# Performance work log

Measured on AMD Instinct MI355X. Metric: run time of the kernel, lower is better.

The kernel has to match this reference:

```python
import jax, jax.numpy as jnp
import numpy as np

B, T, C, H = 2, 2048, 1024, 16
D = C // H  # head dim


def setup_inputs() -> dict:
    key = jax.random.key(0)
    ks = jax.random.split(key, 10)
    s = 1.0 / np.sqrt(C)  # xavier-ish scale
    inp = {
        "q": jax.random.normal(ks[0], (B, T, C), jnp.float32),
        "k": jax.random.normal(ks[1], (B, T, C), jnp.float32),
        "Wq": jax.random.normal(ks[2], (C, C), jnp.float32) * s,
        "bq": jnp.zeros((C,), jnp.float32),
        "Wk": jax.random.normal(ks[3], (C, C), jnp.float32) * s,
        "bk": jnp.zeros((C,), jnp.float32),
        "Wv": jax.random.normal(ks[4], (C, C), jnp.float32) * s,
        "bv": jnp.zeros((C,), jnp.float32),
        "Wo": jax.random.normal(ks[5], (C, C), jnp.float32) * s,
        "bo": jnp.zeros((C,), jnp.float32),
        # causal mask (lower triangular); masked_fill where mask == 0
        "mask": jnp.tril(jnp.ones((T, T), jnp.int32))[None, None],
    }
    return inp


def reference(q, k, Wq, bq, Wk, bk, Wv, bv, Wo, bo, mask):
    # projections (weights stored input-major: y = x @ W + b)
    qp = q @ Wq + bq                       # [B,T,C]
    kp = k @ Wk + bk                       # [B,T,C]
    vp = kp @ Wv + bv                      # quirk: V computed from projected K

    def heads(x):
        return x.reshape(B, T, H, D).transpose(0, 2, 1, 3)  # [B,H,T,D]

    qh, kh, vh = heads(qp), heads(kp), heads(vp)
    scores = jnp.einsum("bhqd,bhkd->bhqk", qh, kh) / jnp.sqrt(jnp.float32(D))
    scores = jnp.where(mask == 0, -jnp.inf, scores)
    attention_weights = jax.nn.softmax(scores, axis=-1)  # [B,H,T,T]
    # dropout omitted (eval mode / p=0)
    ctx = jnp.einsum("bhqk,bhkd->bhqd", attention_weights, vh)
    ctx = ctx.transpose(0, 2, 1, 3).reshape(B, T, C)
    out = ctx @ Wo + bo
    return out, attention_weights
```

## Files before the change

kernel.cpp:

```cpp
#include <hip/hip_runtime.h>

typedef __attribute__((ext_vector_type(8))) short bf16x8;
typedef __attribute__((ext_vector_type(4))) float f32x4;
typedef unsigned short u16;
typedef unsigned int u32;

#define T_SEQ 2048
#define C_DIM 1024
#define NH 16
#define HD 64
#define BATCH 2

__device__ __forceinline__ u16 f2bf(float f) {
    union { float f; u32 u; } v; v.f = f;
    u32 u = v.u;
    u32 r = (u + 0x7FFFu + ((u >> 16) & 1u)) >> 16;
    return (u16)r;
}

__device__ __forceinline__ float fexp2(float x) { return __builtin_amdgcn_exp2f(x); }

__device__ __forceinline__ float bflo(u32 u) {
    union { u32 u; float f; } v; v.u = u << 16; return v.f;
}
__device__ __forceinline__ float bfhi(u32 u) {
    union { u32 u; float f; } v; v.u = u & 0xFFFF0000u; return v.f;
}

__device__ __forceinline__ void gld_lds16(const void* g, void* l) {
    __builtin_amdgcn_global_load_lds(
        (const __attribute__((address_space(1))) void*)g,
        (__attribute__((address_space(3))) void*)l, 16, 0, 0);
}

__global__ __launch_bounds__(256) void transpose_to_bf16(
    const float* __restrict__ W0, const float* __restrict__ W1,
    const float* __restrict__ W2, const float* __restrict__ W3,
    u16* __restrict__ O0, u16* __restrict__ O1,
    u16* __restrict__ O2, u16* __restrict__ O3)
{
    __shared__ float tile[32][33];
    const float* W = blockIdx.z == 0 ? W0 : blockIdx.z == 1 ? W1 : blockIdx.z == 2 ? W2 : W3;
    u16* O = blockIdx.z == 0 ? O0 : blockIdx.z == 1 ? O1 : blockIdx.z == 2 ? O2 : O3;
    const int tx = threadIdx.x, ty = threadIdx.y;
    const int bx = blockIdx.x * 32, by = blockIdx.y * 32;
#pragma unroll
    for (int i = 0; i < 4; ++i)
        tile[ty + i * 8][tx] = W[(size_t)(by + ty + i * 8) * C_DIM + bx + tx];
    __syncthreads();
#pragma unroll
    for (int i = 0; i < 4; ++i)
        O[(size_t)(bx + ty + i * 8) * C_DIM + by + tx] = f2bf(tile[tx][ty + i * 8]);
}

template<bool XF32, int OMODE>
__global__ __launch_bounds__(256) void gemm_bt(
    const void* __restrict__ X0_, const void* __restrict__ X1_,
    const u16* __restrict__ W0T, const u16* __restrict__ W1T,
    const float* __restrict__ b0_, const float* __restrict__ b1_,
    void* __restrict__ Y0_, void* __restrict__ Y1_,
    int M, int N, int K)
{
    __shared__ u16 As[64 * 32];
    __shared__ u16 Bs[128 * 32];
    const int tid = threadIdx.x;
    const int w = tid >> 6, l = tid & 63;
    const int lr = l & 15, lg = l >> 4;
    const int z = blockIdx.z;
    const void* Xv = z ? X1_ : X0_;
    const u16* WT = z ? W1T : W0T;
    const float* bias = z ? b1_ : b0_;
    void* Yv = z ? Y1_ : Y0_;
    const int m0 = blockIdx.y * 64, n0 = blockIdx.x * 128;
    const int grow = l >> 2, gcol = (l & 3) * 8;
    f32x4 acc[4][2] = {};

    for (int k0 = 0; k0 < K; k0 += 32) {
        __syncthreads();
        if (XF32) {
            const int row = tid >> 2, cg = tid & 3;
            const float* g = (const float*)Xv + (size_t)(m0 + row) * K + k0 + cg * 8;
            float4 a0 = *(const float4*)g;
            float4 a1 = *(const float4*)(g + 4);
            union { u16 h[8]; uint4 q; } pk;
            pk.h[0] = f2bf(a0.x); pk.h[1] = f2bf(a0.y);
            pk.h[2] = f2bf(a0.z); pk.h[3] = f2bf(a0.w);
            pk.h[4] = f2bf(a1.x); pk.h[5] = f2bf(a1.y);
            pk.h[6] = f2bf(a1.z); pk.h[7] = f2bf(a1.w);
            *(uint4*)&As[row * 32 + cg * 8] = pk.q;
        } else {
            gld_lds16((const u16*)Xv + (size_t)(m0 + w * 16 + grow) * K + k0 + gcol,
                      &As[w * 512]);
        }
#pragma unroll
        for (int i = 0; i < 2; ++i)
            gld_lds16(WT + (size_t)(n0 + w * 32 + i * 16 + grow) * K + k0 + gcol,
                      &Bs[(w * 2 + i) * 512]);
        __syncthreads();
        bf16x8 af[4], bfr[2];
#pragma unroll
        for (int i = 0; i < 4; ++i)
            af[i] = *(const bf16x8*)&As[(i * 16 + lr) * 32 + lg * 8];
#pragma unroll
        for (int j = 0; j < 2; ++j)
            bfr[j] = *(const bf16x8*)&Bs[(w * 32 + j * 16 + lr) * 32 + lg * 8];
#pragma unroll
        for (int i = 0; i < 4; ++i)
#pragma unroll
            for (int j = 0; j < 2; ++j)
                acc[i][j] = __builtin_amdgcn_mfma_f32_16x16x32_bf16(af[i], bfr[j], acc[i][j], 0, 0, 0);
    }

#pragma unroll
    for (int i = 0; i < 4; ++i) {
        const int rowb = m0 + i * 16 + lg * 4;
#pragma unroll
        for (int j = 0; j < 2; ++j) {
            const int col = n0 + w * 32 + j * 16 + lr;
            const float bv = bias[col];
            if (OMODE == 2) {
                union { u16 h[4]; uint2 q; } pk;
#pragma unroll
                for (int r = 0; r < 4; ++r) pk.h[r] = f2bf(acc[i][j][r] + bv);
                const int bb = rowb >> 11, tt = rowb & 2047;
                const int hh = col >> 6, dd = col & 63;
                u16* dst = (u16*)Yv + ((size_t)((bb * NH + hh) * HD + dd)) * T_SEQ + tt;
                *(uint2*)dst = pk.q;
            } else {
#pragma unroll
                for (int r = 0; r < 4; ++r) {
                    const float v = acc[i][j][r] + bv;
                    if (OMODE == 1)
                        ((float*)Yv)[(size_t)(rowb + r) * N + col] = v;
                    else
                        ((u16*)Yv)[(size_t)(rowb + r) * N + col] = f2bf(v);
                }
            }
        }
    }
}

#define PV_QS 67
#define PV_WS (16 * PV_QS + 8)

__global__ __launch_bounds__(512, 4) void attn_kernel(
    const u16* __restrict__ qp, const u16* __restrict__ kp,
    const u16* __restrict__ vt, u16* __restrict__ ctx,
    float* __restrict__ attn)
{
    __shared__ float statm[8][16], statl[8][16];
    __shared__ float pvbuf[8 * PV_WS];

    const int tid = threadIdx.x;
    const int w = tid >> 6, l = tid & 63;
    const int lr = l & 15, lg = l >> 4;

    const int wgid = (blockIdx.x & 7) * 512 + (blockIdx.x >> 3);
    const int b = wgid >> 11;
    const int h = (wgid >> 7) & 15;
    const int strip = 127 - (wgid & 127);
    const int q0 = strip * 16;

    const size_t bh_off = (size_t)b * T_SEQ * C_DIM + h * HD;
    const u16* qb = qp + bh_off;
    const u16* kb = kp + bh_off;
    const u16* vtb = vt + ((size_t)(b * NH + h) * HD) * T_SEQ;
    float* ab = attn + (size_t)(b * NH + h) * T_SEQ * T_SEQ;

    const float SC = 0.125f * 1.44269504088896f;
    const float MNEG = -1e30f;

    const int qrow = q0 + lr;
    const int n32 = (q0 + 47) >> 5;

    {
        const int zs = n32 * 32;
        const int row = tid >> 5;
        const int c0 = (tid & 31) * 4;
        float* zr = ab + (size_t)(q0 + row) * T_SEQ;
        const f32x4 z4 = { 0.f, 0.f, 0.f, 0.f };
        for (int c = zs + c0; c < T_SEQ; c += 128)
            __builtin_nontemporal_store(z4, (f32x4*)(zr + c));
    }

    const bf16x8 aq0 = *(const bf16x8*)(qb + (size_t)(q0 + lr) * C_DIM + lg * 8);
    const bf16x8 aq1 = *(const bf16x8*)(qb + (size_t)(q0 + lr) * C_DIM + 32 + lg * 8);

    u32 ec[8][2];
    u32 ec2[8][2];
    float mtj[8], Sj[8];
    float ml = MNEG;
#pragma unroll
    for (int j = 0; j < 8; ++j) {
        const int ti = w + 8 * j;
        if (ti < n32) {
            const int kvb = ti * 32;
            const u16* kr0 = kb + (size_t)(kvb + lr) * C_DIM;
            const u16* kr1 = kb + (size_t)(kvb + 16 + lr) * C_DIM;
            const bf16x8 k00 = *(const bf16x8*)(kr0 + lg * 8);
            const bf16x8 k01 = *(const bf16x8*)(kr0 + 32 + lg * 8);
            const bf16x8 k10 = *(const bf16x8*)(kr1 + lg * 8);
            const bf16x8 k11 = *(const bf16x8*)(kr1 + 32 + lg * 8);
            f32x4 s[2] = {};
            s[0] = __builtin_amdgcn_mfma_f32_16x16x32_bf16(k00, aq0, s[0], 0, 0, 0);
            s[0] = __builtin_amdgcn_mfma_f32_16x16x32_bf16(k01, aq1, s[0], 0, 0, 0);
            s[1] = __builtin_amdgcn_mfma_f32_16x16x32_bf16(k10, aq0, s[1], 0, 0, 0);
            s[1] = __builtin_amdgcn_mfma_f32_16x16x32_bf16(k11, aq1, s[1], 0, 0, 0);
            float sv[2][4];
            float mt = MNEG;
#pragma unroll
            for (int t = 0; t < 2; ++t)
#pragma unroll
                for (int r = 0; r < 4; ++r) {
                    float v = s[t][r] * SC;
                    if (kvb + 16 * t + 4 * lg + r > qrow) v = MNEG;
                    sv[t][r] = v;
                    mt = fmaxf(mt, v);
                }
            mtj[j] = mt;
            float ss = 0.f;
            float e[2][4];
#pragma unroll
            for (int t = 0; t < 2; ++t)
#pragma unroll
                for (int r = 0; r < 4; ++r) {
                    e[t][r] = fexp2(sv[t][r] - mt);
                    ss += e[t][r];
                }
            Sj[j] = ss;
#pragma unroll
            for (int t = 0; t < 2; ++t) {
                ec[j][t]  = (u32)f2bf(e[t][0]) | ((u32)f2bf(e[t][1]) << 16);
                ec2[j][t] = (u32)f2bf(e[t][2]) | ((u32)f2bf(e[t][3]) << 16);
            }
            ml = fmaxf(ml, mt);
        } else {
            mtj[j] = MNEG; Sj[j] = 0.f;
            ec[j][0] = ec[j][1] = ec2[j][0] = ec2[j][1] = 0;
        }
    }
    float ll = 0.f;
#pragma unroll
    for (int j = 0; j < 8; ++j) ll += Sj[j] * fexp2(mtj[j] - ml);
#pragma unroll
    for (int d = 16; d <= 32; d <<= 1) {
        const float mo = __shfl_xor(ml, d);
        const float lo = __shfl_xor(ll, d);
        const float mn = fmaxf(ml, mo);
        ll = ll * fexp2(ml - mn) + lo * fexp2(mo - mn);
        ml = mn;
    }
    if (l < 16) { statm[w][lr] = ml; statl[w][lr] = ll; }
    __syncthreads();

    float mf = MNEG;
#pragma unroll
    for (int ww = 0; ww < 8; ++ww) mf = fmaxf(mf, statm[ww][lr]);
    float lf = 0.f;
#pragma unroll
    for (int ww = 0; ww < 8; ++ww) lf += statl[ww][lr] * fexp2(statm[ww][lr] - mf);
    const float rlf = 1.f / lf;

    f32x4 cacc[4] = {};
#pragma unroll
    for (int j = 0; j < 8; ++j) {
        const int ti = w + 8 * j;
        if (ti < n32) {
            const int kvb = ti * 32;
            bf16x8 vf[4];
#pragma unroll
            for (int dt = 0; dt < 4; ++dt)
                vf[dt] = *(const bf16x8*)(vtb + (size_t)(dt * 16 + lr) * T_SEQ + kvb + lg * 8);
            const float scale = fexp2(mtj[j] - mf) * rlf;
            u32 pw[2][2];
#pragma unroll
            for (int t2 = 0; t2 < 2; ++t2) {
                float p[4];
                p[0] = bflo(ec[j][t2]) * scale;
                p[1] = bfhi(ec[j][t2]) * scale;
                p[2] = bflo(ec2[j][t2]) * scale;
                p[3] = bfhi(ec2[j][t2]) * scale;
                f32x4 pv4 = { p[0], p[1], p[2], p[3] };
                __builtin_nontemporal_store(pv4,
                    (f32x4*)(ab + (size_t)qrow * T_SEQ + kvb + 16 * t2 + 4 * lg));
                pw[t2][0] = (u32)f2bf(p[0]) | ((u32)f2bf(p[1]) << 16);
                pw[t2][1] = (u32)f2bf(p[2]) | ((u32)f2bf(p[3]) << 16);
            }
            const int bl = lr + ((lg & 1) << 5);
            const u32 a0 = (u32)__shfl((int)pw[0][0], bl);
            const u32 a1 = (u32)__shfl((int)pw[0][1], bl);
            const u32 a2 = (u32)__shfl((int)pw[0][0], bl + 16);
            const u32 a3 = (u32)__shfl((int)pw[0][1], bl + 16);
            const u32 b0 = (u32)__shfl((int)pw[1][0], bl);
            const u32 b1 = (u32)__shfl((int)pw[1][1], bl);
            const u32 b2 = (u32)__shfl((int)pw[1][0], bl + 16);
            const u32 b3 = (u32)__shfl((int)pw[1][1], bl + 16);
            const bool hi2 = lg >= 2;
            union { u32 ww[4]; bf16x8 v; } pa;
            pa.ww[0] = hi2 ? b0 : a0;
            pa.ww[1] = hi2 ? b1 : a1;
            pa.ww[2] = hi2 ? b2 : a2;
            pa.ww[3] = hi2 ? b3 : a3;
            __builtin_amdgcn_s_setprio(1);
#pragma unroll
            for (int dt = 0; dt < 4; ++dt)
                cacc[dt] = __builtin_amdgcn_mfma_f32_16x16x32_bf16(pa.v, vf[dt], cacc[dt], 0, 0, 0);
            __builtin_amdgcn_s_setprio(0);
        }
    }

    {
        float* pwv = pvbuf + w * PV_WS;
#pragma unroll
        for (int dt = 0; dt < 4; ++dt)
#pragma unroll
            for (int r = 0; r < 4; ++r)
                pwv[(4 * lg + r) * PV_QS + dt * 16 + lr] = cacc[dt][r];
    }
    __syncthreads();

    {
        const int qq = tid >> 5;
        const int d0 = (tid & 31) * 2;
        float s0 = 0.f, s1 = 0.f;
#pragma unroll
        for (int ww = 0; ww < 8; ++ww) {
            const float* pwv = pvbuf + ww * PV_WS + qq * PV_QS;
            s0 += pwv[d0];
            s1 += pwv[d0 + 1];
        }
        union { u16 hh[2]; u32 u; } pk;
        pk.hh[0] = f2bf(s0); pk.hh[1] = f2bf(s1);
        u16* cb = ctx + bh_off;
        *(u32*)(cb + (size_t)(q0 + qq) * C_DIM + d0) = pk.u;
    }
}

extern "C" void kernel_launch(void* const* d_in, const int* in_sizes, int n_in,
                              void* d_out, int out_size, void* d_ws, size_t ws_size,
                              hipStream_t stream)
{
    const float* q  = (const float*)d_in[0];
    const float* k  = (const float*)d_in[1];
    const float* Wq = (const float*)d_in[2];
    const float* bq = (const float*)d_in[3];
    const float* Wk = (const float*)d_in[4];
    const float* bk = (const float*)d_in[5];
    const float* Wv = (const float*)d_in[6];
    const float* bv = (const float*)d_in[7];
    const float* Wo = (const float*)d_in[8];
    const float* bo = (const float*)d_in[9];
    (void)in_sizes; (void)n_in; (void)out_size; (void)ws_size;

    float* out = (float*)d_out;
    float* attn = out + (size_t)BATCH * T_SEQ * C_DIM;

    const size_t MC = (size_t)BATCH * T_SEQ * C_DIM;
    u16* qp  = (u16*)d_ws;
    u16* kp  = qp + MC;
    u16* vt  = kp + MC;
    u16* ctx = vt + MC;
    u16* WqT = ctx + MC;
    u16* WkT = WqT + (size_t)C_DIM * C_DIM;
    u16* WvT = WkT + (size_t)C_DIM * C_DIM;
    u16* WoT = WvT + (size_t)C_DIM * C_DIM;

    transpose_to_bf16<<<dim3(32, 32, 4), dim3(32, 8), 0, stream>>>(
        Wq, Wk, Wv, Wo, WqT, WkT, WvT, WoT);

    const int M = BATCH * T_SEQ;
    dim3 gqk(C_DIM / 128, M / 64, 2);
    dim3 g1(C_DIM / 128, M / 64, 1);
    gemm_bt<true, 0><<<gqk, 256, 0, stream>>>(q, k, WqT, WkT, bq, bk,
                                              qp, kp, M, C_DIM, C_DIM);
    gemm_bt<false, 2><<<g1, 256, 0, stream>>>(kp, kp, WvT, WvT, bv, bv,
                                              vt, vt, M, C_DIM, C_DIM);

    attn_kernel<<<dim3(4096), 512, 0, stream>>>(qp, kp, vt, ctx, attn);

    gemm_bt<false, 1><<<g1, 256, 0, stream>>>(ctx, ctx, WoT, WoT, bo, bo,
                                              out, out, M, C_DIM, C_DIM);
}
```

Baseline: 254.2 us.

## Double-buffer LDS tiles and widen K-step to 64 in projection GEMM

The projection GEMM now keeps two LDS buffers for the A and B tiles and uses a K-step of 64 instead of 32. The next tile is issued to global (or global-to-LDS) loads before the MFMAs on the current tile, so memory latency overlaps compute, and only one barrier is needed per iteration. This doubles LDS use per block, which may cut occupancy. The wider rows also change the LDS access pattern, which could add bank conflicts on the fragment reads.

Result: slower. 264.7 us (+4.2%).

```diff
diff --git a/kernel.cpp b/kernel.cpp
--- a/kernel.cpp
+++ b/kernel.cpp
@@ -61,8 +61,8 @@
     void* __restrict__ Y0_, void* __restrict__ Y1_,
     int M, int N, int K)
 {
-    __shared__ u16 As[64 * 32];
-    __shared__ u16 Bs[128 * 32];
+    __shared__ u16 As[2][64 * 64];
+    __shared__ u16 Bs[2][128 * 64];
     const int tid = threadIdx.x;
     const int w = tid >> 6, l = tid & 63;
     const int lr = l & 15, lg = l >> 4;
@@ -72,43 +72,85 @@
     const float* bias = z ? b1_ : b0_;
     void* Yv = z ? Y1_ : Y0_;
     const int m0 = blockIdx.y * 64, n0 = blockIdx.x * 128;
-    const int grow = l >> 2, gcol = (l & 3) * 8;
+    const int grow8 = l >> 3;
+    const int gcol8 = (l & 7) * 8;
+    const int rowA = tid >> 2, cgA = tid & 3;
     f32x4 acc[4][2] = {};
 
-    for (int k0 = 0; k0 < K; k0 += 32) {
+    auto stageB = [&](int k0, int buf) {
+#pragma unroll
+        for (int i = 0; i < 4; ++i)
+            gld_lds16(WT + (size_t)(n0 + w * 32 + i * 8 + grow8) * K + k0 + gcol8,
+                      &Bs[buf][(w * 32 + i * 8) * 64]);
+    };
+    auto stageAb = [&](int k0, int buf) {
+#pragma unroll
+        for (int i = 0; i < 2; ++i)
+            gld_lds16((const u16*)Xv + (size_t)(m0 + w * 16 + i * 8 + grow8) * K + k0 + gcol8,
+                      &As[buf][(w * 16 + i * 8) * 64]);
+    };
+
+    if (XF32) {
+        const float* g = (const float*)Xv + (size_t)(m0 + rowA) * K + cgA * 16;
+        float4 a0 = *(const float4*)g;
+        float4 a1 = *(const float4*)(g + 4);
+        float4 a2 = *(const float4*)(g + 8);
+        float4 a3 = *(const float4*)(g + 12);
+        union { u16 h[8]; uint4 q; } p0, p1;
+        p0.h[0] = f2bf(a0.x); p0.h[1] = f2bf(a0.y); p0.h[2] = f2bf(a0.z); p0.h[3] = f2bf(a0.w);
+        p0.h[4] = f2bf(a1.x); p0.h[5] = f2bf(a1.y); p0.h[6] = f2bf(a1.z); p0.h[7] = f2bf(a1.w);
+        p1.h[0] = f2bf(a2.x); p1.h[1] = f2bf(a2.y); p1.h[2] = f2bf(a2.z); p1.h[3] = f2bf(a2.w);
+        p1.h[4] = f2bf(a3.x); p1.h[5] = f2bf(a3.y); p1.h[6] = f2bf(a3.z); p1.h[7] = f2bf(a3.w);
+        *(uint4*)&As[0][rowA * 64 + cgA * 16] = p0.q;
+        *(uint4*)&As[0][rowA * 64 + cgA * 16 + 8] = p1.q;
+    } else {
+        stageAb(0, 0);
+    }
+    stageB(0, 0);
+    __syncthreads();
+
+    int cur = 0;
+    for (int k0 = 0; k0 < K; k0 += 64) {
+        const bool has_next = (k0 + 64 < K);
+        float4 a0, a1, a2, a3;
+        if (has_next) {
+            if (XF32) {
+                const float* g = (const float*)Xv + (size_t)(m0 + rowA) * K + k0 + 64 + cgA * 16;
+                a0 = *(const float4*)g;
+                a1 = *(const float4*)(g + 4);
+                a2 = *(const float4*)(g + 8);
+                a3 = *(const float4*)(g + 12);
+            } else {
+                stageAb(k0 + 64, cur ^ 1);
+            }
+            stageB(k0 + 64, cur ^ 1);
+        }
+#pragma unroll
+        for (int h = 0; h < 2; ++h) {
+            bf16x8 af[4], bfr[2];
+#pragma unroll
+            for (int i = 0; i < 4; ++i)
+                af[i] = *(const bf16x8*)&As[cur][(i * 16 + lr) * 64 + h * 32 + lg * 8];
+#pragma unroll
+            for (int j = 0; j < 2; ++j)
+                bfr[j] = *(const bf16x8*)&Bs[cur][(w * 32 + j * 16 + lr) * 64 + h * 32 + lg * 8];
+#pragma unroll
+            for (int i = 0; i < 4; ++i)
+#pragma unroll
+                for (int j = 0; j < 2; ++j)
+                    acc[i][j] = __builtin_amdgcn_mfma_f32_16x16x32_bf16(af[i], bfr[j], acc[i][j], 0, 0, 0);
+        }
+        if (XF32 && has_next) {
+            union { u16 h[8]; uint4 q; } p0, p1;
+            p0.h[0] = f2bf(a0.x); p0.h[1] = f2bf(a0.y); p0.h[2] = f2bf(a0.z); p0.h[3] = f2bf(a0.w);
+            p0.h[4] = f2bf(a1.x); p0.h[5] = f2bf(a1.y); p0.h[6] = f2bf(a1.z); p0.h[7] = f2bf(a1.w);
+            p1.h[0] = f2bf(a2.x); p1.h[1] = f2bf(a2.y); p1.h[2] = f2bf(a2.z); p1.h[3] = f2bf(a2.w);
+            p1.h[4] = f2bf(a3.x); p1.h[5] = f2bf(a3.y); p1.h[6] = f2bf(a3.z); p1.h[7] = f2bf(a3.w);
+            *(uint4*)&As[cur ^ 1][rowA * 64 + cgA * 16] = p0.q;
+            *(uint4*)&As[cur ^ 1][rowA * 64 + cgA * 16 + 8] = p1.q;
+        }
         __syncthreads();
-        if (XF32) {
-            const int row = tid >> 2, cg = tid & 3;
-            const float* g = (const float*)Xv + (size_t)(m0 + row) * K + k0 + cg * 8;
-            float4 a0 = *(const float4*)g;
-            float4 a1 = *(const float4*)(g + 4);
-            union { u16 h[8]; uint4 q; } pk;
-            pk.h[0] = f2bf(a0.x); pk.h[1] = f2bf(a0.y);
-            pk.h[2] = f2bf(a0.z); pk.h[3] = f2bf(a0.w);
-            pk.h[4] = f2bf(a1.x); pk.h[5] = f2bf(a1.y);
-            pk.h[6] = f2bf(a1.z); pk.h[7] = f2bf(a1.w);
-            *(uint4*)&As[row * 32 + cg * 8] = pk.q;
-        } else {
-            gld_lds16((const u16*)Xv + (size_t)(m0 + w * 16 + grow) * K + k0 + gcol,
-                      &As[w * 512]);
-        }
-#pragma unroll
-        for (int i = 0; i < 2; ++i)
-            gld_lds16(WT + (size_t)(n0 + w * 32 + i * 16 + grow) * K + k0 + gcol,
-                      &Bs[(w * 2 + i) * 512]);
-        __syncthreads();
-        bf16x8 af[4], bfr[2];
-#pragma unroll
-        for (int i = 0; i < 4; ++i)
-            af[i] = *(const bf16x8*)&As[(i * 16 + lr) * 32 + lg * 8];
-#pragma unroll
-        for (int j = 0; j < 2; ++j)
-            bfr[j] = *(const bf16x8*)&Bs[(w * 32 + j * 16 + lr) * 32 + lg * 8];
-#pragma unroll
-        for (int i = 0; i < 4; ++i)
-#pragma unroll
-            for (int j = 0; j < 2; ++j)
-                acc[i][j] = __builtin_amdgcn_mfma_f32_16x16x32_bf16(af[i], bfr[j], acc[i][j], 0, 0, 0);
+        cur ^= 1;
     }
 
 #pragma unroll
```

## Stage attention probabilities in LDS for coalesced stores, contiguous tile ranges per wave

Applied to the files above, without the earlier changes.

Each wave now handles a contiguous range of key tiles instead of a strided set. This lets two adjacent 32-column tiles be staged in shared memory and written to the attention matrix as contiguous 256-byte row segments, replacing the earlier scattered 16-byte stores. The goal is to cut the store-transaction overhead on the large fp32 attention-weights output. In exchange it adds LDS traffic, more shared memory per block (which can lower occupancy), and a possibly less even split of work across waves.

Result: no change. 250.2 us (-1.6%).

```diff
diff --git a/kernel.cpp b/kernel.cpp
--- a/kernel.cpp
+++ b/kernel.cpp
@@ -150,6 +150,7 @@
 {
     __shared__ float statm[8][16], statl[8][16];
     __shared__ float pvbuf[8 * PV_WS];
+    __shared__ float pchunk[8][16][68];
 
     const int tid = threadIdx.x;
     const int w = tid >> 6, l = tid & 63;
@@ -171,10 +172,12 @@
     const float MNEG = -1e30f;
 
     const int qrow = q0 + lr;
-    const int n32 = (q0 + 47) >> 5;
+    const int nt = (q0 + 47) >> 5;
+    const int lo = (w * nt) >> 3;
+    const int hi = ((w + 1) * nt) >> 3;
 
     {
-        const int zs = n32 * 32;
+        const int zs = nt * 32;
         const int row = tid >> 5;
         const int c0 = (tid & 31) * 4;
         float* zr = ab + (size_t)(q0 + row) * T_SEQ;
@@ -191,9 +194,9 @@
     float mtj[8], Sj[8];
     float ml = MNEG;
 #pragma unroll
-    for (int j = 0; j < 8; ++j) {
-        const int ti = w + 8 * j;
-        if (ti < n32) {
+    for (int jj = 0; jj < 8; ++jj) {
+        const int ti = lo + jj;
+        if (ti < hi) {
             const int kvb = ti * 32;
             const u16* kr0 = kb + (size_t)(kvb + lr) * C_DIM;
             const u16* kr1 = kb + (size_t)(kvb + 16 + lr) * C_DIM;
@@ -217,7 +220,7 @@
                     sv[t][r] = v;
                     mt = fmaxf(mt, v);
                 }
-            mtj[j] = mt;
+            mtj[jj] = mt;
             float ss = 0.f;
             float e[2][4];
 #pragma unroll
@@ -227,27 +230,27 @@
                     e[t][r] = fexp2(sv[t][r] - mt);
                     ss += e[t][r];
                 }
-            Sj[j] = ss;
+            Sj[jj] = ss;
 #pragma unroll
             for (int t = 0; t < 2; ++t) {
-                ec[j][t]  = (u32)f2bf(e[t][0]) | ((u32)f2bf(e[t][1]) << 16);
-                ec2[j][t] = (u32)f2bf(e[t][2]) | ((u32)f2bf(e[t][3]) << 16);
+                ec[jj][t]  = (u32)f2bf(e[t][0]) | ((u32)f2bf(e[t][1]) << 16);
+                ec2[jj][t] = (u32)f2bf(e[t][2]) | ((u32)f2bf(e[t][3]) << 16);
             }
             ml = fmaxf(ml, mt);
         } else {
-            mtj[j] = MNEG; Sj[j] = 0.f;
-            ec[j][0] = ec[j][1] = ec2[j][0] = ec2[j][1] = 0;
+            mtj[jj] = MNEG; Sj[jj] = 0.f;
+            ec[jj][0] = ec[jj][1] = ec2[jj][0] = ec2[jj][1] = 0;
         }
     }
     float ll = 0.f;
 #pragma unroll
-    for (int j = 0; j < 8; ++j) ll += Sj[j] * fexp2(mtj[j] - ml);
+    for (int jj = 0; jj < 8; ++jj) ll += Sj[jj] * fexp2(mtj[jj] - ml);
 #pragma unroll
     for (int d = 16; d <= 32; d <<= 1) {
         const float mo = __shfl_xor(ml, d);
-        const float lo = __shfl_xor(ll, d);
+        const float lo2 = __shfl_xor(ll, d);
         const float mn = fmaxf(ml, mo);
-        ll = ll * fexp2(ml - mn) + lo * fexp2(mo - mn);
+        ll = ll * fexp2(ml - mn) + lo2 * fexp2(mo - mn);
         ml = mn;
     }
     if (l < 16) { statm[w][lr] = ml; statl[w][lr] = ll; }
@@ -263,49 +266,77 @@
 
     f32x4 cacc[4] = {};
 #pragma unroll
-    for (int j = 0; j < 8; ++j) {
-        const int ti = w + 8 * j;
-        if (ti < n32) {
-            const int kvb = ti * 32;
-            bf16x8 vf[4];
-#pragma unroll
-            for (int dt = 0; dt < 4; ++dt)
-                vf[dt] = *(const bf16x8*)(vtb + (size_t)(dt * 16 + lr) * T_SEQ + kvb + lg * 8);
-            const float scale = fexp2(mtj[j] - mf) * rlf;
-            u32 pw[2][2];
-#pragma unroll
-            for (int t2 = 0; t2 < 2; ++t2) {
-                float p[4];
-                p[0] = bflo(ec[j][t2]) * scale;
-                p[1] = bfhi(ec[j][t2]) * scale;
-                p[2] = bflo(ec2[j][t2]) * scale;
-                p[3] = bfhi(ec2[j][t2]) * scale;
-                f32x4 pv4 = { p[0], p[1], p[2], p[3] };
-                __builtin_nontemporal_store(pv4,
-                    (f32x4*)(ab + (size_t)qrow * T_SEQ + kvb + 16 * t2 + 4 * lg));
-                pw[t2][0] = (u32)f2bf(p[0]) | ((u32)f2bf(p[1]) << 16);
-                pw[t2][1] = (u32)f2bf(p[2]) | ((u32)f2bf(p[3]) << 16);
+    for (int j0 = 0; j0 < 8; j0 += 2) {
+        int nv = 0;
+#pragma unroll
+        for (int c = 0; c < 2; ++c) {
+            const int jj = j0 + c;
+            const int ti = lo + jj;
+            if (ti < hi) {
+                nv = c + 1;
+                const int kvb = ti * 32;
+                bf16x8 vf[4];
+#pragma unroll
+                for (int dt = 0; dt < 4; ++dt)
+                    vf[dt] = *(const bf16x8*)(vtb + (size_t)(dt * 16 + lr) * T_SEQ + kvb + lg * 8);
+                const float scale = fexp2(mtj[jj] - mf) * rlf;
+                u32 pw[2][2];
+#pragma unroll
+                for (int t2 = 0; t2 < 2; ++t2) {
+                    float p[4];
+                    p[0] = bflo(ec[jj][t2]) * scale;
+                    p[1] = bfhi(ec[jj][t2]) * scale;
+                    p[2] = bflo(ec2[jj][t2]) * scale;
+                    p[3] = bfhi(ec2[jj][t2]) * scale;
+                    f32x4 pv4 = { p[0], p[1], p[2], p[3] };
+                    *(f32x4*)&pchunk[w][lr][c * 32 + 16 * t2 + 4 * lg] = pv4;
+                    pw[t2][0] = (u32)f2bf(p[0]) | ((u32)f2bf(p[1]) << 16);
+                    pw[t2][1] = (u32)f2bf(p[2]) | ((u32)f2bf(p[3]) << 16);
+                }
+                const int bl = lr + ((lg & 1) << 5);
+                const u32 a0 = (u32)__shfl((int)pw[0][0], bl);
+                const u32 a1 = (u32)__shfl((int)pw[0][1], bl);
+                const u32 a2 = (u32)__shfl((int)pw[0][0], bl + 16);
+                const u32 a3 = (u32)__shfl((int)pw[0][1], bl + 16);
+                const u32 b0 = (u32)__shfl((int)pw[1][0], bl);
+                const u32 b1 = (u32)__shfl((int)pw[1][1], bl);
+                const u32 b2 = (u32)__shfl((int)pw[1][0], bl + 16);
+                const u32 b3 = (u32)__shfl((int)pw[1][1], bl + 16);
+                const bool hi2 = lg >= 2;
+                union { u32 ww[4]; bf16x8 v; } pa;
+                pa.ww[0] = hi2 ? b0 : a0;
+                pa.ww[1] = hi2 ? b1 : a1;
+                pa.ww[2] = hi2 ? b2 : a2;
+                pa.ww[3] = hi2 ? b3 : a3;
+                __builtin_amdgcn_s_setprio(1);
+#pragma unroll
+                for (int dt = 0; dt < 4; ++dt)
+                    cacc[dt] = __builtin_amdgcn_mfma_f32_16x16x32_bf16(pa.v, vf[dt], cacc[dt], 0, 0, 0);
+                __builtin_amdgcn_s_setprio(0);
             }
-            const int bl = lr + ((lg & 1) << 5);
-            const u32 a0 = (u32)__shfl((int)pw[0][0], bl);
-            const u32 a1 = (u32)__shfl((int)pw[0][1], bl);
-            const u32 a2 = (u32)__shfl((int)pw[0][0], bl + 16);
-            const u32 a3 = (u32)__shfl((int)pw[0][1], bl + 16);
-            const u32 b0 = (u32)__shfl((int)pw[1][0], bl);
-            const u32 b1 = (u32)__shfl((int)pw[1][1], bl);
-            const u32 b2 = (u32)__shfl((int)pw[1][0], bl + 16);
-            const u32 b3 = (u32)__shfl((int)pw[1][1], bl + 16);
-            const bool hi2 = lg >= 2;
-            union { u32 ww[4]; bf16x8 v; } pa;
-            pa.ww[0] = hi2 ? b0 : a0;
-            pa.ww[1] = hi2 ? b1 : a1;
-            pa.ww[2] = hi2 ? b2 : a2;
-            pa.ww[3] = hi2 ? b3 : a3;
-            __builtin_amdgcn_s_setprio(1);
-#pragma unroll
-            for (int dt = 0; dt < 4; ++dt)
-                cacc[dt] = __builtin_amdgcn_mfma_f32_16x16x32_bf16(pa.v, vf[dt], cacc[dt], 0, 0, 0);
-            __builtin_amdgcn_s_setprio(0);
+        }
+        if (nv) {
+            asm volatile("s_waitcnt lgkmcnt(0)" ::: "memory");
+            const int colbase = (lo + j0) * 32;
+            if (nv == 2) {
+#pragma unroll
+                for (int i = 0; i < 4; ++i) {
+                    const int row = i * 4 + (l >> 4);
+                    const int col = (l & 15) * 4;
+                    const f32x4 v = *(const f32x4*)&pchunk[w][row][col];
+                    __builtin_nontemporal_store(v,
+                        (f32x4*)(ab + (size_t)(q0 + row) * T_SEQ + colbase + col));
+                }
+            } else {
+#pragma unroll
+                for (int i = 0; i < 2; ++i) {
+                    const int row = i * 8 + (l >> 3);
+                    const int col = (l & 7) * 4;
+                    const f32x4 v = *(const f32x4*)&pchunk[w][row][col];
+                    __builtin_nontemporal_store(v,
+                        (f32x4*)(ab + (size_t)(q0 + row) * T_SEQ + colbase + col));
+                }
+            }
         }
     }
 
```
